# Kernel tuning notes

Hardware: AMD Instinct MI355X
Metric: run time of the kernel (lower is better)

## Reference

```python
import jax, jax.numpy as jnp
import numpy as np

B, D, P, K, L_S = 512, 1024, 64, 16, 16


def _make_M():
    # fixed signed mask: top-left PxP block = -1, bottom-left KxP block = +1
    M = np.zeros((P + K, P + K), dtype=np.float32)
    M[:P, :P] = -1.0
    M[P:, :P] = +1.0
    return jnp.asarray(M)


def setup_inputs() -> dict:
    key = jax.random.key(0)
    k1, k2, k3 = jax.random.split(key, 3)
    X_tilde = jax.random.normal(k1, (B, D, P + K), dtype=jnp.float32)
    y_train = jax.random.normal(k2, (B, P), dtype=jnp.float32)
    gamma = jax.random.normal(k3, (D,), dtype=jnp.float32) * 0.01
    return {"X_tilde": X_tilde, "y_train": y_train, "gamma": gamma}


def reference(X_tilde, y_train, gamma):
    M = _make_M()  # [P+K, P+K]
    Bsz = X_tilde.shape[0]
    # h0 = [y_train, 0_K]  -> [B, P+K]
    h0 = jnp.concatenate([y_train, jnp.zeros((Bsz, K), dtype=y_train.dtype)], axis=-1)
    # score[b,m,n] = sum_d gamma[d] * X[b,d,m] * X[b,d,n] / P
    weighted = gamma[None, :, None] * X_tilde  # [B, D, P+K]
    score = jnp.einsum('bdm,bdn->bmn', weighted, X_tilde) / float(P)
    masked_score = M[None, :, :] * score  # [B, P+K, P+K]
    inv_L = 1.0 / float(L_S)

    def step(h, _):
        h = h + inv_L * jnp.einsum('bmn,bn->bm', masked_score, h)
        return h, None

    h, _ = jax.lax.scan(step, h0, None, length=L_S)
    return h[:, P:]
```

## Files before the change

### kernel.cpp

```cpp
#include <hip/hip_runtime.h>


namespace {
typedef __attribute__((ext_vector_type(8))) short bf16x8;
typedef __attribute__((ext_vector_type(4))) float f32x4;
typedef __attribute__((ext_vector_type(4))) float fv4;
typedef __attribute__((ext_vector_type(2))) unsigned uv2;

constexpr int kB  = 512;
constexpr int kD  = 1024;
constexpr int kP  = 64;
constexpr int kKK = 16;
constexpr int kLS = 16;
constexpr int kThreads = 320;
constexpr int kKc = 64;
constexpr int kNC = kD / kKc;

constexpr int TB    = 4096;
constexpr int ASZ   = 80 * 64 * 2;
constexpr int BSZ   = 64 * 64 * 2;
constexpr int BUFSZ = ASZ + BSZ;
constexpr int LDS_BYTES = TB + 2 * BUFSZ;

__device__ __forceinline__ unsigned short bf16_bits(float x) {
  unsigned u = __builtin_bit_cast(unsigned, x);
  u += 0x7fffu + ((u >> 16) & 1u);
  return (unsigned short)(u >> 16);
}
__device__ __forceinline__ unsigned bpack(float lo, float hi) {
  return (unsigned)bf16_bits(lo) | ((unsigned)bf16_bits(hi) << 16);
}

__global__ void __launch_bounds__(kThreads)
tcsf_kernel(const float* __restrict__ X, const float* __restrict__ y,
            const float* __restrict__ gamma, float* __restrict__ out) {
  __shared__ __align__(16) char smem[LDS_BYTES];
  float* gs = reinterpret_cast<float*>(smem);

  const int t = threadIdx.x;
  const int b = blockIdx.x;
  const int l = t & 63;
  const int w = t >> 6;

  for (int i = t; i < kD; i += kThreads) gs[i] = gamma[i];

  const fv4* Xg = reinterpret_cast<const fv4*>(X) + (size_t)b * (kD * 80 / 4);

  const int ct = t % 20;
  const int kt = t / 20;

  f32x4 acc[4];
#pragma unroll
  for (int nt = 0; nt < 4; ++nt) acc[nt] = (f32x4)(0.f);

  fv4 v0, v1, v2, v3;
  fv4 g4;

  __syncthreads();

  {
    const int base = (0 * kKc + 4 * kt) * 20 + ct;
    v0 = Xg[base]; v1 = Xg[base + 20]; v2 = Xg[base + 40]; v3 = Xg[base + 60];
    g4 = *reinterpret_cast<const fv4*>(gs + 0 * kKc + 4 * kt);
    char* Ab = smem + TB;
    char* Bb = Ab + ASZ;
#pragma unroll
    for (int j = 0; j < 4; ++j) {
      const int m = 4 * ct + j;
      const int rowo = m * 128;
      const int col = (8 * kt) ^ ((m & 7) << 4);
      uv2 wa; wa.x = bpack(v0[j], v1[j]); wa.y = bpack(v2[j], v3[j]);
      *reinterpret_cast<uv2*>(Ab + rowo + col) = wa;
      if (ct < 16) {
        uv2 wb; wb.x = bpack(g4[0] * v0[j], g4[1] * v1[j]);
        wb.y = bpack(g4[2] * v2[j], g4[3] * v3[j]);
        *reinterpret_cast<uv2*>(Bb + rowo + col) = wb;
      }
    }
  }

  const int rA = 16 * w + (l & 15);
  const int colb = (l >> 4) * 16;
  const int fswz = (l & 7) << 4;

  for (int c = 0; c < kNC; ++c) {
    if (c + 1 < kNC) {
      const int base = ((c + 1) * kKc + 4 * kt) * 20 + ct;
      v0 = Xg[base]; v1 = Xg[base + 20]; v2 = Xg[base + 40]; v3 = Xg[base + 60];
      g4 = *reinterpret_cast<const fv4*>(gs + (c + 1) * kKc + 4 * kt);
    }
    __syncthreads();
    {
      const char* Ab = smem + TB + (c & 1) * BUFSZ;
      const char* Bb = Ab + ASZ;
#pragma unroll
      for (int ks = 0; ks < 2; ++ks) {
        const int cb = ks * 64 + colb;
        const bf16x8 a = *reinterpret_cast<const bf16x8*>(Ab + rA * 128 + (cb ^ fswz));
#pragma unroll
        for (int nt = 0; nt < 4; ++nt) {
          const bf16x8 bb = *reinterpret_cast<const bf16x8*>(
              Bb + (16 * nt + (l & 15)) * 128 + (cb ^ fswz));
          acc[nt] = __builtin_amdgcn_mfma_f32_16x16x32_bf16(a, bb, acc[nt], 0, 0, 0);
        }
      }
    }
    __syncthreads();
    if (c + 1 < kNC) {
      char* Ab = smem + TB + ((c + 1) & 1) * BUFSZ;
      char* Bb = Ab + ASZ;
#pragma unroll
      for (int j = 0; j < 4; ++j) {
        const int m = 4 * ct + j;
        const int rowo = m * 128;
        const int col = (8 * kt) ^ ((m & 7) << 4);
        uv2 wa; wa.x = bpack(v0[j], v1[j]); wa.y = bpack(v2[j], v3[j]);
        *reinterpret_cast<uv2*>(Ab + rowo + col) = wa;
        if (ct < 16) {
          uv2 wb; wb.x = bpack(g4[0] * v0[j], g4[1] * v1[j]);
          wb.y = bpack(g4[2] * v2[j], g4[3] * v3[j]);
          *reinterpret_cast<uv2*>(Bb + rowo + col) = wb;
        }
      }
    }
  }

  float* Gl = reinterpret_cast<float*>(smem + TB);
  float* hp = Gl + 80 * 65;
  constexpr float invP = 1.0f / 64.0f;
#pragma unroll
  for (int nt = 0; nt < 4; ++nt)
#pragma unroll
    for (int r = 0; r < 4; ++r)
      Gl[(16 * w + (l >> 4) * 4 + r) * 65 + 16 * nt + (l & 15)] = acc[nt][r] * invP;

  if (t < kP) hp[t] = y[b * kP + t];
  __syncthreads();

  const int m = t >> 2;
  const int part = t & 3;
  const float* Grow = Gl + m * 65 + part * 16;
  const float* hpp = hp + part * 16;
  float hk = 0.f;
  constexpr float invL = 1.0f / kLS;
  for (int s = 0; s < kLS; ++s) {
    float d0 = 0.f, d1 = 0.f, d2 = 0.f, d3 = 0.f;
#pragma unroll
    for (int i = 0; i < 16; i += 4) {
      d0 = fmaf(Grow[i + 0], hpp[i + 0], d0);
      d1 = fmaf(Grow[i + 1], hpp[i + 1], d1);
      d2 = fmaf(Grow[i + 2], hpp[i + 2], d2);
      d3 = fmaf(Grow[i + 3], hpp[i + 3], d3);
    }
    float dot = (d0 + d1) + (d2 + d3);
    dot += __shfl_xor(dot, 1);
    dot += __shfl_xor(dot, 2);
    __syncthreads();
    if (part == 0) {
      if (m < kP) hp[m] -= invL * dot;
      else        hk   += invL * dot;
    }
    __syncthreads();
  }
  if (part == 0 && m >= kP) out[b * kKK + (m - kP)] = hk;
}

}

extern "C" void kernel_launch(void* const* d_in, const int* in_sizes, int n_in,
                              void* d_out, int out_size, void* d_ws, size_t ws_size,
                              hipStream_t stream) {
  const float* X     = (const float*)d_in[0];
  const float* y     = (const float*)d_in[1];
  const float* gamma = (const float*)d_in[2];
  float* out = (float*)d_out;
  tcsf_kernel<<<dim3(kB), dim3(kThreads), 0, stream>>>(X, y, gamma, out);
}
```

Baseline: 39.77 us.

## Double thread count, split K across two warp groups, ping-pong h buffer

The block grows to 640 threads in two groups of 5 waves. Each group computes MFMA over one half of each 128-wide K slice. The groups take turns loading global data two chunks ahead and staging the next chunk into LDS, so only one barrier is needed per chunk. The partial Gram results are combined through LDS, and the recurrence now uses 8 threads per row with a double-buffered h, which removes one barrier per step. Costs are more registers per block, possibly fewer resident blocks, and an extra LDS reduction pass.

Result: slower. 41.30 us (+3.9%).

```diff
diff --git a/kernel.cpp b/kernel.cpp
--- a/kernel.cpp
+++ b/kernel.cpp
@@ -12,7 +12,7 @@
 constexpr int kP  = 64;
 constexpr int kKK = 16;
 constexpr int kLS = 16;
-constexpr int kThreads = 320;
+constexpr int kThreads = 640;
 constexpr int kKc = 64;
 constexpr int kNC = kD / kKc;
 
@@ -41,29 +41,36 @@
   const int b = blockIdx.x;
   const int l = t & 63;
   const int w = t >> 6;
+  const int grp = (w >= 5) ? 1 : 0;
+  const int slab = grp ? (w - 5) : w;
+  const int tg = grp ? (t - 320) : t;
+  const int ct = tg % 20;
+  const int kt = tg / 20;
 
   for (int i = t; i < kD; i += kThreads) gs[i] = gamma[i];
 
   const fv4* Xg = reinterpret_cast<const fv4*>(X) + (size_t)b * (kD * 80 / 4);
-
-  const int ct = t % 20;
-  const int kt = t / 20;
 
   f32x4 acc[4];
 #pragma unroll
   for (int nt = 0; nt < 4; ++nt) acc[nt] = (f32x4)(0.f);
 
   fv4 v0, v1, v2, v3;
-  fv4 g4;
 
-  __syncthreads();
+  const int rA   = 16 * slab + (l & 15);
+  const int cb   = grp * 64 + (l >> 4) * 16;
+  const int fswz = (l & 7) << 4;
 
   {
-    const int base = (0 * kKc + 4 * kt) * 20 + ct;
+    const int c0 = grp;
+    const int base = (c0 * kKc + 4 * kt) * 20 + ct;
     v0 = Xg[base]; v1 = Xg[base + 20]; v2 = Xg[base + 40]; v3 = Xg[base + 60];
-    g4 = *reinterpret_cast<const fv4*>(gs + 0 * kKc + 4 * kt);
+  }
+  __syncthreads();
+  if (grp == 0) {
     char* Ab = smem + TB;
     char* Bb = Ab + ASZ;
+    const fv4 g4 = *reinterpret_cast<const fv4*>(gs + 4 * kt);
 #pragma unroll
     for (int j = 0; j < 4; ++j) {
       const int m = 4 * ct + j;
@@ -78,37 +85,18 @@
       }
     }
   }
-
-  const int rA = 16 * w + (l & 15);
-  const int colb = (l >> 4) * 16;
-  const int fswz = (l & 7) << 4;
+  __syncthreads();
 
   for (int c = 0; c < kNC; ++c) {
-    if (c + 1 < kNC) {
-      const int base = ((c + 1) * kKc + 4 * kt) * 20 + ct;
+    const int pl = c & 1;
+    if (c + 2 < kNC && grp == pl) {
+      const int base = ((c + 2) * kKc + 4 * kt) * 20 + ct;
       v0 = Xg[base]; v1 = Xg[base + 20]; v2 = Xg[base + 40]; v3 = Xg[base + 60];
-      g4 = *reinterpret_cast<const fv4*>(gs + (c + 1) * kKc + 4 * kt);
     }
-    __syncthreads();
-    {
-      const char* Ab = smem + TB + (c & 1) * BUFSZ;
-      const char* Bb = Ab + ASZ;
-#pragma unroll
-      for (int ks = 0; ks < 2; ++ks) {
-        const int cb = ks * 64 + colb;
-        const bf16x8 a = *reinterpret_cast<const bf16x8*>(Ab + rA * 128 + (cb ^ fswz));
-#pragma unroll
-        for (int nt = 0; nt < 4; ++nt) {
-          const bf16x8 bb = *reinterpret_cast<const bf16x8*>(
-              Bb + (16 * nt + (l & 15)) * 128 + (cb ^ fswz));
-          acc[nt] = __builtin_amdgcn_mfma_f32_16x16x32_bf16(a, bb, acc[nt], 0, 0, 0);
-        }
-      }
-    }
-    __syncthreads();
-    if (c + 1 < kNC) {
+    if (c + 1 < kNC && grp != pl) {
       char* Ab = smem + TB + ((c + 1) & 1) * BUFSZ;
       char* Bb = Ab + ASZ;
+      const fv4 g4 = *reinterpret_cast<const fv4*>(gs + (c + 1) * kKc + 4 * kt);
 #pragma unroll
       for (int j = 0; j < 4; ++j) {
         const int m = 4 * ct + j;
@@ -123,30 +111,54 @@
         }
       }
     }
+    {
+      const char* Ab = smem + TB + pl * BUFSZ;
+      const char* Bb = Ab + ASZ;
+      const bf16x8 a = *reinterpret_cast<const bf16x8*>(Ab + rA * 128 + (cb ^ fswz));
+#pragma unroll
+      for (int nt = 0; nt < 4; ++nt) {
+        const bf16x8 bb = *reinterpret_cast<const bf16x8*>(
+            Bb + (16 * nt + (l & 15)) * 128 + (cb ^ fswz));
+        acc[nt] = __builtin_amdgcn_mfma_f32_16x16x32_bf16(a, bb, acc[nt], 0, 0, 0);
+      }
+    }
+    __syncthreads();
   }
 
   float* Gl = reinterpret_cast<float*>(smem + TB);
   float* hp = Gl + 80 * 65;
   constexpr float invP = 1.0f / 64.0f;
+  if (grp) {
 #pragma unroll
-  for (int nt = 0; nt < 4; ++nt)
+    for (int nt = 0; nt < 4; ++nt)
 #pragma unroll
-    for (int r = 0; r < 4; ++r)
-      Gl[(16 * w + (l >> 4) * 4 + r) * 65 + 16 * nt + (l & 15)] = acc[nt][r] * invP;
-
+      for (int r = 0; r < 4; ++r)
+        Gl[(16 * slab + (l >> 4) * 4 + r) * 65 + 16 * nt + (l & 15)] = acc[nt][r];
+  }
+  __syncthreads();
+  if (!grp) {
+#pragma unroll
+    for (int nt = 0; nt < 4; ++nt)
+#pragma unroll
+      for (int r = 0; r < 4; ++r) {
+        const int idx = (16 * slab + (l >> 4) * 4 + r) * 65 + 16 * nt + (l & 15);
+        Gl[idx] = (Gl[idx] + acc[nt][r]) * invP;
+      }
+  }
   if (t < kP) hp[t] = y[b * kP + t];
   __syncthreads();
 
-  const int m = t >> 2;
-  const int part = t & 3;
-  const float* Grow = Gl + m * 65 + part * 16;
-  const float* hpp = hp + part * 16;
+  const int m = t >> 3;
+  const int part = t & 7;
+  const float* Grow = Gl + m * 65 + part * 8;
   float hk = 0.f;
   constexpr float invL = 1.0f / kLS;
   for (int s = 0; s < kLS; ++s) {
+    const float* hpc = hp + (s & 1) * kP;
+    const float* hpp = hpc + part * 8;
     float d0 = 0.f, d1 = 0.f, d2 = 0.f, d3 = 0.f;
 #pragma unroll
-    for (int i = 0; i < 16; i += 4) {
+    for (int i = 0; i < 8; i += 4) {
       d0 = fmaf(Grow[i + 0], hpp[i + 0], d0);
       d1 = fmaf(Grow[i + 1], hpp[i + 1], d1);
       d2 = fmaf(Grow[i + 2], hpp[i + 2], d2);
@@ -155,10 +167,10 @@
     float dot = (d0 + d1) + (d2 + d3);
     dot += __shfl_xor(dot, 1);
     dot += __shfl_xor(dot, 2);
-    __syncthreads();
+    dot += __shfl_xor(dot, 4);
     if (part == 0) {
-      if (m < kP) hp[m] -= invL * dot;
-      else        hk   += invL * dot;
+      if (m < kP) hp[((s + 1) & 1) * kP + m] = hpc[m] - invL * dot;
+      else        hk += invL * dot;
     }
     __syncthreads();
   }
```
